# Performance work log

Measured on AMD Instinct MI355X. Metric: run time of the kernel, lower is better.

The kernel has to match this reference:

```python
import jax, jax.numpy as jnp
import numpy as np

N_SITES = 4096
NUM_TYPES = 3
INTERACTION_ORDER = 4
BATCH = 64


def _make_symmetric(t):
    # symmetrize over the two type axes (alpha, beta)
    return (t + jnp.transpose(t, (1, 0, 2))) / 2.0


def setup_inputs() -> dict:
    key = jax.random.key(0)
    k1, k2, k3 = jax.random.split(key, 3)
    interaction = _make_symmetric(
        jax.random.uniform(k1, (NUM_TYPES, NUM_TYPES, INTERACTION_ORDER), dtype=jnp.float32)
    )
    adjacency = jax.random.uniform(
        k2, (N_SITES, N_SITES, INTERACTION_ORDER), dtype=jnp.float32
    )
    v_batch = jax.random.normal(k3, (N_SITES, NUM_TYPES, BATCH), dtype=jnp.float32)
    return {
        "interaction_tensor": interaction,
        "adjacency_tensor": adjacency,
        "v_batch": v_batch,
    }


def reference(interaction_tensor, adjacency_tensor, v_batch):
    # E_s = 0.5 * sum_{a,b,n,i,j} W[a,b,n] * A[i,j,n] * v[i,a,s] * v[j,b,s]
    # Contract the big adjacency against v first so the (i,j,a,b) intermediate
    # is never materialized: A(ijn) x v(jbs) -> t(inbs) is the only O(N^2) step.
    t = jnp.einsum('ijn,jbs->inbs', adjacency_tensor, v_batch)  # [N, n, T, S]
    out = 0.5 * jnp.einsum('inbs,ias,abn->s', t, v_batch, interaction_tensor)
    return out
```

## Files before the change

### kernel.cpp

```cpp
#include <hip/hip_runtime.h>
#include <hip/hip_bf16.h>


typedef __attribute__((ext_vector_type(8))) short short8;
typedef __attribute__((ext_vector_type(4))) float floatx4;

#define VF_U4 (12*512*16)
#define NBLK  512

__device__ __forceinline__ unsigned short f2bf(float f) {
    union { float f; unsigned u; } x; x.f = f;
    unsigned r = x.u + 0x7fffu + ((x.u >> 16) & 1u);
    return (unsigned short)(r >> 16);
}
__device__ __forceinline__ unsigned pack2(float lo, float hi) {
    return (unsigned)f2bf(lo) | ((unsigned)f2bf(hi) << 16);
}

__global__ void prep_vfrag(const float* __restrict__ v, uint4* __restrict__ vf) {
    int tid = blockIdx.x * 256 + threadIdx.x;
    if (tid >= VF_U4) return;
    int ci = tid & 15;
    int kb = (tid >> 4) & 511;
    int f  = tid >> 13;
    int c = f * 16 + ci;
    int b = c >> 6, s = c & 63;
    int j0 = kb * 8;
    unsigned q0 = pack2(v[((j0+0)*3+b)*64+s], v[((j0+1)*3+b)*64+s]);
    unsigned q1 = pack2(v[((j0+2)*3+b)*64+s], v[((j0+3)*3+b)*64+s]);
    unsigned q2 = pack2(v[((j0+4)*3+b)*64+s], v[((j0+5)*3+b)*64+s]);
    unsigned q3 = pack2(v[((j0+6)*3+b)*64+s], v[((j0+7)*3+b)*64+s]);
    vf[tid] = make_uint4(q0, q1, q2, q3);
}

__global__ __launch_bounds__(512, 4) void energy_main(
        const float* __restrict__ A, const float* __restrict__ v,
        const float* __restrict__ W, const uint4* __restrict__ vf,
        float* __restrict__ partials) {
    __shared__ __align__(16) unsigned As32[4096];
    __shared__ float Wl[36];
    __shared__ float El[64];

    const int tid = threadIdx.x;
    const int bid = blockIdx.x;
    const int ib = bid >> 1, jh = bid & 1;
    const int i0 = ib * 16;
    const int jbase = jh * 2048;

    if (tid < 36) Wl[tid] = W[tid];
    if (tid < 64) El[tid] = 0.0f;

    const int lane = tid & 63;
    const int w = tid >> 6;
    const int kh = w >> 2;
    const int ws = w & 3;

    const int r  = tid >> 5;
    const int jp = tid & 31;
    const long arowBase = (long)(i0 + r) * 4096 + jbase + 2 * jp;
    const int aWrIdx = r * 32 + (((jp >> 2) ^ (r & 7)) << 2) + (jp & 3);

    const int rr = lane & 15;
    const int gA = (kh * 4 + (lane >> 4)) ^ (rr & 7);
    const int aRdOff = rr * 128 + gA * 16;

    const int kbBase = (jbase + kh * 32) >> 3;

    floatx4 acc[4][3];
    #pragma unroll
    for (int n = 0; n < 4; ++n)
        #pragma unroll
        for (int cf = 0; cf < 3; ++cf)
            #pragma unroll
            for (int q = 0; q < 4; ++q) acc[n][cf][q] = 0.0f;

    const float4* A4 = reinterpret_cast<const float4*>(A);

    {
        float4 a0 = A4[arowBase];
        float4 a1 = A4[arowBase + 1];
        As32[0*512 + aWrIdx] = pack2(a0.x, a1.x);
        As32[1*512 + aWrIdx] = pack2(a0.y, a1.y);
        As32[2*512 + aWrIdx] = pack2(a0.z, a1.z);
        As32[3*512 + aWrIdx] = pack2(a0.w, a1.w);
    }
    short8 bc[3];
    #pragma unroll
    for (int cf = 0; cf < 3; ++cf)
        bc[cf] = *reinterpret_cast<const short8*>(vf + ((ws*3+cf)*512 + kbBase)*16 + lane);

    int cur = 0;
    for (int t = 0; t < 32; ++t) {
        __syncthreads();
        float4 na0, na1;
        short8 bn[3];
        if (t < 31) {
            long o = arowBase + (long)(t + 1) * 64;
            na0 = A4[o];
            na1 = A4[o + 1];
            int kb = kbBase + (t + 1) * 8;
            #pragma unroll
            for (int cf = 0; cf < 3; ++cf)
                bn[cf] = *reinterpret_cast<const short8*>(vf + ((ws*3+cf)*512 + kb)*16 + lane);
        }
        const char* ab = reinterpret_cast<const char*>(As32) + cur * 8192 + aRdOff;
        short8 af[4];
        #pragma unroll
        for (int n = 0; n < 4; ++n)
            af[n] = *reinterpret_cast<const short8*>(ab + n * 2048);
        #pragma unroll
        for (int n = 0; n < 4; ++n)
            #pragma unroll
            for (int cf = 0; cf < 3; ++cf)
                acc[n][cf] = __builtin_amdgcn_mfma_f32_16x16x32_bf16(
                    af[n], bc[cf], acc[n][cf], 0, 0, 0);
        __syncthreads();
        if (t < 31) {
            const int base = (cur ^ 1) * 2048 + aWrIdx;
            As32[base + 0*512] = pack2(na0.x, na1.x);
            As32[base + 1*512] = pack2(na0.y, na1.y);
            As32[base + 2*512] = pack2(na0.z, na1.z);
            As32[base + 3*512] = pack2(na0.w, na1.w);
            bc[0] = bn[0]; bc[1] = bn[1]; bc[2] = bn[2];
        }
        cur ^= 1;
    }

    float cont[3];
    #pragma unroll
    for (int cf = 0; cf < 3; ++cf) {
        int c = ws * 48 + cf * 16 + rr;
        int b = c >> 6, s = c & 63;
        float sum = 0.0f;
        #pragma unroll
        for (int rg = 0; rg < 4; ++rg) {
            int i = i0 + (lane >> 4) * 4 + rg;
            float v0 = v[(i * 3 + 0) * 64 + s];
            float v1 = v[(i * 3 + 1) * 64 + s];
            float v2 = v[(i * 3 + 2) * 64 + s];
            #pragma unroll
            for (int n = 0; n < 4; ++n) {
                float P = Wl[b * 4 + n] * v0 + Wl[12 + b * 4 + n] * v1
                        + Wl[24 + b * 4 + n] * v2;
                sum += acc[n][cf][rg] * P;
            }
        }
        cont[cf] = sum;
    }
    #pragma unroll
    for (int cf = 0; cf < 3; ++cf) {
        cont[cf] += __shfl_xor(cont[cf], 16);
        cont[cf] += __shfl_xor(cont[cf], 32);
    }
    __syncthreads();
    if (lane < 16) {
        #pragma unroll
        for (int cf = 0; cf < 3; ++cf) {
            int s = (ws * 48 + cf * 16 + lane) & 63;
            atomicAdd(&El[s], cont[cf]);
        }
    }
    __syncthreads();
    if (tid < 64) partials[bid * 64 + tid] = 0.5f * El[tid];
}

__global__ void reduce_out(const float* __restrict__ partials, float* __restrict__ out) {
    int s = threadIdx.x;
    float a = 0.0f;
    for (int b = 0; b < NBLK; ++b) a += partials[b * 64 + s];
    out[s] = a;
}

extern "C" void kernel_launch(void* const* d_in, const int* in_sizes, int n_in,
                              void* d_out, int out_size, void* d_ws, size_t ws_size,
                              hipStream_t stream) {
    const float* W = (const float*)d_in[0];
    const float* A = (const float*)d_in[1];
    const float* v = (const float*)d_in[2];
    float* out = (float*)d_out;
    uint4* vf = (uint4*)d_ws;
    float* partials = (float*)((char*)d_ws + (size_t)VF_U4 * 16);

    hipLaunchKernelGGL(prep_vfrag, dim3((VF_U4 + 255) / 256), dim3(256), 0, stream, v, vf);
    hipLaunchKernelGGL(energy_main, dim3(NBLK), dim3(512), 0, stream, A, v, W, vf, partials);
    hipLaunchKernelGGL(reduce_out, dim3(1), dim3(64), 0, stream, partials, out);
}
```

Baseline: 76.41 us.

## Deepen A prefetch to two tiles, use one barrier per step, parallelize final reduce

The main loop now keeps the next A tile in registers two iterations ahead, loaded with nontemporal loads, and writes it to the alternate LDS buffer before the MFMAs, so one __syncthreads per iteration suffices instead of two. This is meant to hide more HBM latency for the streamed 256MB adjacency tensor and to cut barrier stalls. The final reduction kernel goes from 64 to 512 threads with an LDS combine, shortening its serial loop over 512 partials. The change costs extra registers for the in-flight A data, which may lower occupancy under the 512x4 launch bound.

```diff
diff --git a/kernel.cpp b/kernel.cpp
--- a/kernel.cpp
+++ b/kernel.cpp
@@ -74,55 +74,58 @@
             #pragma unroll
             for (int q = 0; q < 4; ++q) acc[n][cf][q] = 0.0f;
 
-    const float4* A4 = reinterpret_cast<const float4*>(A);
+    const floatx4* A4 = reinterpret_cast<const floatx4*>(A);
 
     {
-        float4 a0 = A4[arowBase];
-        float4 a1 = A4[arowBase + 1];
+        floatx4 a0 = __builtin_nontemporal_load(A4 + arowBase);
+        floatx4 a1 = __builtin_nontemporal_load(A4 + arowBase + 1);
         As32[0*512 + aWrIdx] = pack2(a0.x, a1.x);
         As32[1*512 + aWrIdx] = pack2(a0.y, a1.y);
         As32[2*512 + aWrIdx] = pack2(a0.z, a1.z);
         As32[3*512 + aWrIdx] = pack2(a0.w, a1.w);
     }
+    floatx4 rA0 = __builtin_nontemporal_load(A4 + arowBase + 64);
+    floatx4 rA1 = __builtin_nontemporal_load(A4 + arowBase + 65);
     short8 bc[3];
     #pragma unroll
     for (int cf = 0; cf < 3; ++cf)
         bc[cf] = *reinterpret_cast<const short8*>(vf + ((ws*3+cf)*512 + kbBase)*16 + lane);
+    __syncthreads();
 
     int cur = 0;
     for (int t = 0; t < 32; ++t) {
-        __syncthreads();
-        float4 na0, na1;
+        const char* ab = reinterpret_cast<const char*>(As32) + cur * 8192 + aRdOff;
+        short8 af[4];
+        #pragma unroll
+        for (int n = 0; n < 4; ++n)
+            af[n] = *reinterpret_cast<const short8*>(ab + n * 2048);
+        if (t < 31) {
+            const int base = (cur ^ 1) * 2048 + aWrIdx;
+            As32[base + 0*512] = pack2(rA0.x, rA1.x);
+            As32[base + 1*512] = pack2(rA0.y, rA1.y);
+            As32[base + 2*512] = pack2(rA0.z, rA1.z);
+            As32[base + 3*512] = pack2(rA0.w, rA1.w);
+        }
+        if (t < 30) {
+            long o = arowBase + (long)(t + 2) * 64;
+            rA0 = __builtin_nontemporal_load(A4 + o);
+            rA1 = __builtin_nontemporal_load(A4 + o + 1);
+        }
         short8 bn[3];
         if (t < 31) {
-            long o = arowBase + (long)(t + 1) * 64;
-            na0 = A4[o];
-            na1 = A4[o + 1];
             int kb = kbBase + (t + 1) * 8;
             #pragma unroll
             for (int cf = 0; cf < 3; ++cf)
                 bn[cf] = *reinterpret_cast<const short8*>(vf + ((ws*3+cf)*512 + kb)*16 + lane);
         }
-        const char* ab = reinterpret_cast<const char*>(As32) + cur * 8192 + aRdOff;
-        short8 af[4];
-        #pragma unroll
-        for (int n = 0; n < 4; ++n)
-            af[n] = *reinterpret_cast<const short8*>(ab + n * 2048);
         #pragma unroll
         for (int n = 0; n < 4; ++n)
             #pragma unroll
             for (int cf = 0; cf < 3; ++cf)
                 acc[n][cf] = __builtin_amdgcn_mfma_f32_16x16x32_bf16(
                     af[n], bc[cf], acc[n][cf], 0, 0, 0);
+        if (t < 31) { bc[0] = bn[0]; bc[1] = bn[1]; bc[2] = bn[2]; }
         __syncthreads();
-        if (t < 31) {
-            const int base = (cur ^ 1) * 2048 + aWrIdx;
-            As32[base + 0*512] = pack2(na0.x, na1.x);
-            As32[base + 1*512] = pack2(na0.y, na1.y);
-            As32[base + 2*512] = pack2(na0.z, na1.z);
-            As32[base + 3*512] = pack2(na0.w, na1.w);
-            bc[0] = bn[0]; bc[1] = bn[1]; bc[2] = bn[2];
-        }
         cur ^= 1;
     }
 
@@ -165,10 +168,20 @@
 }
 
 __global__ void reduce_out(const float* __restrict__ partials, float* __restrict__ out) {
-    int s = threadIdx.x;
+    __shared__ float red[8][64];
+    int tid = threadIdx.x;
+    int chunk = tid >> 6, s = tid & 63;
     float a = 0.0f;
-    for (int b = 0; b < NBLK; ++b) a += partials[b * 64 + s];
-    out[s] = a;
+    for (int m = 0; m < NBLK / 8; ++m)
+        a += partials[((m << 3) + chunk) * 64 + s];
+    red[chunk][s] = a;
+    __syncthreads();
+    if (tid < 64) {
+        float t = 0.0f;
+        #pragma unroll
+        for (int c = 0; c < 8; ++c) t += red[c][tid];
+        out[tid] = t;
+    }
 }
 
 extern "C" void kernel_launch(void* const* d_in, const int* in_sizes, int n_in,
@@ -183,5 +196,5 @@
 
     hipLaunchKernelGGL(prep_vfrag, dim3((VF_U4 + 255) / 256), dim3(256), 0, stream, v, vf);
     hipLaunchKernelGGL(energy_main, dim3(NBLK), dim3(512), 0, stream, A, v, W, vf, partials);
-    hipLaunchKernelGGL(reduce_out, dim3(1), dim3(64), 0, stream, partials, out);
-}
+    hipLaunchKernelGGL(reduce_out, dim3(1), dim3(512), 0, stream, partials, out);
+}
```

After: 80.40 us. +5.2%, slower.
